# Kernel tuning notes

Hardware: AMD Instinct MI355X
Metric: run time of the kernel (lower is better)

The kernel has to match this reference:

```python
import jax, jax.numpy as jnp
import numpy as np

N = 16384          # nodes
E = 262144         # edges (avg degree 16)
MUL0, MUL1 = 16, 8 # multiplicities of 0e and 1o irreps
DIM = MUL0 + 3 * MUL1  # 40
NB, RH = 10, 16    # radial basis size, radial hidden
MAX_RADIUS = 1.3
W00_N = MUL0 * MUL0
W11_N = MUL1 * MUL0
W01_N = MUL0 * MUL1
W10_N = MUL1 * MUL1
WNUM = W00_N + W11_N + W01_N + W10_N  # 576
INV_SQRT3 = 1.0 / np.sqrt(3.0)        # wigner-3j (1,1,0) / (1,0,1) factor
A_PATH = 1.0 / np.sqrt(MUL0 + MUL1)   # path/fan normalization


def split_irreps(x):
    sc = x[..., :MUL0]
    vec = x[..., MUL0:].reshape(x.shape[:-1] + (MUL1, 3))
    return sc, vec


def radial_net(emb, w1, w2):
    h = jax.nn.silu(emb @ w1 / np.sqrt(NB))
    return h @ w2 / np.sqrt(RH)  # [E, WNUM]


def fc_tp(f_sc, f_vec, sh_sc, sh_vec, w):
    # fully-connected tensor product (input irreps x SH -> output irreps), per-edge weights
    w00 = w[:, :W00_N].reshape(-1, MUL0, MUL0)
    w11 = w[:, W00_N:W00_N + W11_N].reshape(-1, MUL1, MUL0)
    w01 = w[:, W00_N + W11_N:W00_N + W11_N + W01_N].reshape(-1, MUL0, MUL1)
    w10 = w[:, -W10_N:].reshape(-1, MUL1, MUL1)
    out_sc = A_PATH * (jnp.einsum('ei,e,eio->eo', f_sc, sh_sc, w00)
                       + INV_SQRT3 * jnp.einsum('eic,ec,eio->eo', f_vec, sh_vec, w11))
    out_vec = A_PATH * (jnp.einsum('ei,ec,eio->eoc', f_sc, sh_vec, w01)
                        + jnp.einsum('eic,e,eio->eoc', f_vec, sh_sc, w10))
    return out_sc, out_vec


def dot_tp(q_sc, q_vec, k_sc, k_vec, Wd00, Wd11):
    # FullyConnectedTensorProduct(query, key, '0e') with shared weights -> scalar per edge
    s0 = jnp.einsum('ei,ej,ij->e', q_sc, k_sc, Wd00) / MUL0
    s1 = jnp.einsum('eic,ejc,ij->e', q_vec, k_vec, Wd11) / (MUL1 * np.sqrt(3.0))
    return (s0 + s1) / np.sqrt(2.0)


def soft_unit_step(x):
    xs = jnp.where(x > 0, x, 1.0)
    return jnp.where(x > 0, jnp.exp(-1.0 / xs), 0.0)


def setup_inputs():
    key = jax.random.key(0)
    ks = jax.random.split(key, 13)
    return {
        'f': jax.random.normal(ks[0], (N, DIM), jnp.float32),
        'edge_index': jax.random.randint(ks[1], (2, E), 0, N),
        'edge_length': jax.random.uniform(ks[2], (E,), jnp.float32),
        'edge_sh': jax.random.normal(ks[3], (E, 4), jnp.float32),
        'edge_length_embedded': jax.random.uniform(ks[4], (E, NB), jnp.float32),
        'Wq0': jax.random.normal(ks[5], (MUL0, MUL0), jnp.float32),
        'Wq1': jax.random.normal(ks[6], (MUL1, MUL1), jnp.float32),
        'fck_w1': jax.random.normal(ks[7], (NB, RH), jnp.float32),
        'fck_w2': jax.random.normal(ks[8], (RH, WNUM), jnp.float32),
        'fcv_w1': jax.random.normal(ks[9], (NB, RH), jnp.float32),
        'fcv_w2': jax.random.normal(ks[10], (RH, WNUM), jnp.float32),
        'Wd00': jax.random.normal(ks[11], (MUL0, MUL0), jnp.float32),
        'Wd11': jax.random.normal(ks[12], (MUL1, MUL1), jnp.float32),
    }


def reference(f, edge_index, edge_length, edge_sh, edge_length_embedded,
              Wq0, Wq1, fck_w1, fck_w2, fcv_w1, fcv_w2, Wd00, Wd11):
    f_sc, f_vec = split_irreps(f)
    # h_q: equivariant linear (per-irrep channel mixing)
    q_sc = f_sc @ Wq0 / np.sqrt(MUL0)
    q_vec = jnp.einsum('nic,io->noc', f_vec, Wq1) / np.sqrt(MUL1)
    src, dst = edge_index[0], edge_index[1]
    sh_sc, sh_vec = edge_sh[:, 0], edge_sh[:, 1:4]
    # radial MLPs -> per-edge TP weights
    wk = radial_net(edge_length_embedded, fck_w1, fck_w2)
    wv = radial_net(edge_length_embedded, fcv_w1, fcv_w2)
    k_sc, k_vec = fc_tp(f_sc[dst], f_vec[dst], sh_sc, sh_vec, wk)
    v_sc, v_vec = fc_tp(f_sc[src], f_vec[src], sh_sc, sh_vec, wv)
    cut = soft_unit_step(10.0 * (1.0 - edge_length / MAX_RADIUS))
    s = dot_tp(q_sc[dst], q_vec[dst], k_sc, k_vec, Wd00, Wd11)
    exp_ijk = cut * jnp.exp(s)                                   # [E]
    z = jax.ops.segment_sum(exp_ijk, dst, num_segments=N)        # [N]
    z = jnp.where(z == 0, 1.0, z)
    alpha = exp_ijk / z[dst]
    w_edge = jnp.sqrt(jnp.maximum(alpha, 0.0))[:, None]          # sqrt(relu(alpha))
    v_flat = jnp.concatenate([v_sc, v_vec.reshape(-1, MUL1 * 3)], axis=-1)
    f_out = jax.ops.segment_sum(w_edge * v_flat, dst, num_segments=N)
    return f_out
```

## Files before the change

### kernel.cpp

```cpp
#include <hip/hip_runtime.h>
#include <hip/hip_bf16.h>
#include <math.h>

namespace {
constexpr int NN  = 16384;
constexpr int NE  = 262144;
constexpr int DIM = 40;

constexpr float INV_SQRT3   = 0.5773502691896258f;
constexpr float A_PATH      = 0.2041241452319315f;
constexpr float INV_SQRT_NB = 0.31622776601683794f;
constexpr float H_SCALE     = 0.25f;
constexpr float QSC_S       = 0.25f;
constexpr float QV_S        = 0.35355339059327373f;
constexpr float D00_S       = 1.0f / (16.0f * 1.4142135623730951f);
constexpr float D11_S       = 1.0f / (8.0f * 1.7320508075688772f * 1.4142135623730951f);

constexpr int BKP = 392;
constexpr int K0P = 328;
constexpr int KCP = 264;
constexpr int BKTOT = 16 * K0P + 16 * KCP;
constexpr int FEP = 40;

constexpr int PREP_NODE_BLKS = NN / 256;
constexpr int PREP_BV_BLKS   = 32 * BKP / 256;
constexpr int PREP_BK_BLKS   = BKTOT / 256;
}

typedef __attribute__((ext_vector_type(8))) _Float16 f16x8;
typedef __attribute__((ext_vector_type(4))) float f32x4;

static __device__ __forceinline__ void gload_lds16(const void* g, void* l) {
  __builtin_amdgcn_global_load_lds(
      (const __attribute__((address_space(1))) unsigned*)g,
      (__attribute__((address_space(3))) unsigned*)l, 16, 0, 0);
}

__global__ __launch_bounds__(256) void prep_kernel(
    const float* __restrict__ f,
    const float* __restrict__ Wq0, const float* __restrict__ Wq1,
    const float* __restrict__ Wd00, const float* __restrict__ Wd11,
    const float* __restrict__ w2v,
    const float* __restrict__ w2k,
    float* __restrict__ qd,
    unsigned short* __restrict__ Btv,
    unsigned short* __restrict__ Btk,
    int* __restrict__ cnt)
{
  const int blk = blockIdx.x;
  if (blk < PREP_NODE_BLKS) {
    const int n = blk * 256 + threadIdx.x;
    cnt[n] = 0;

    float fs[16], fv[8][3];
    {
      const float4* fn4 = reinterpret_cast<const float4*>(f + (size_t)n * DIM);
#pragma unroll
      for (int i = 0; i < 10; i++) {
        float4 t = fn4[i];
        int base = i * 4;
#pragma unroll
        for (int k = 0; k < 4; k++) {
          float v = (k == 0) ? t.x : (k == 1) ? t.y : (k == 2) ? t.z : t.w;
          int idx = base + k;
          if (idx < 16) fs[idx] = v;
          else { int r = idx - 16; fv[r / 3][r % 3] = v; }
        }
      }
    }

    float out[40];
    {
      float qsc[16];
#pragma unroll
      for (int o = 0; o < 16; o++) {
        float a = 0.f;
#pragma unroll
        for (int i = 0; i < 16; i++) a += fs[i] * Wq0[i * 16 + o];
        qsc[o] = a * QSC_S;
      }
#pragma unroll
      for (int j = 0; j < 16; j++) {
        float a = 0.f;
#pragma unroll
        for (int i = 0; i < 16; i++) a += qsc[i] * Wd00[i * 16 + j];
        out[j] = a * D00_S;
      }
    }
    {
      float qv[8][3];
#pragma unroll
      for (int o = 0; o < 8; o++)
#pragma unroll
        for (int c = 0; c < 3; c++) {
          float a = 0.f;
#pragma unroll
          for (int i = 0; i < 8; i++) a += fv[i][c] * Wq1[i * 8 + o];
          qv[o][c] = a * QV_S;
        }
#pragma unroll
      for (int j = 0; j < 8; j++)
#pragma unroll
        for (int c = 0; c < 3; c++) {
          float a = 0.f;
#pragma unroll
          for (int i = 0; i < 8; i++) a += qv[i][c] * Wd11[i * 8 + j];
          out[16 + j * 3 + c] = a * D11_S;
        }
    }

    float4* op = reinterpret_cast<float4*>(qd + (size_t)n * DIM);
#pragma unroll
    for (int i = 0; i < 10; i++)
      op[i] = make_float4(out[4 * i], out[4 * i + 1], out[4 * i + 2], out[4 * i + 3]);

  } else if (blk < PREP_NODE_BLKS + PREP_BV_BLKS) {
    int t = (blk - PREP_NODE_BLKS) * 256 + threadIdx.x;
    int col = t / BKP, kp = t % BKP;
    float val = 0.f;
    if (kp < 384 && col < 24) {
      if (kp < 256) {
        int r = kp >> 4, i = kp & 15;
        if (col < 16) val = A_PATH * w2v[r * 576 + i * 16 + col];
        else          val = A_PATH * w2v[r * 576 + 384 + i * 8 + (col - 16)];
      } else {
        int k2 = kp - 256; int r = k2 >> 3, i = k2 & 7;
        if (col < 16) val = A_PATH * INV_SQRT3 * w2v[r * 576 + 256 + i * 16 + col];
        else          val = A_PATH * w2v[r * 576 + 512 + i * 8 + (col - 16)];
      }
    }
    _Float16 hv = (_Float16)val;
    Btv[t] = __builtin_bit_cast(unsigned short, hv);

  } else {
    int t = (blk - PREP_NODE_BLKS - PREP_BV_BLKS) * 256 + threadIdx.x;
    float val = 0.f;
    if (t < 16 * K0P) {
      int r = t / K0P, k = t % K0P;
      if (k < 256)      { int i = k >> 4, o = k & 15; val = w2k[r * 576 + i * 16 + o]; }
      else if (k < 320) { int kk = k - 256; int i = kk >> 3, o = kk & 7;
                          val = w2k[r * 576 + 512 + i * 8 + o]; }
    } else {
      int t2 = t - 16 * K0P;
      int r = t2 / KCP, k = t2 % KCP;
      if (k < 128)      { int i = k >> 4, o = k & 15;
                          val = INV_SQRT3 * w2k[r * 576 + 256 + i * 16 + o]; }
      else if (k < 256) { int kk = k - 128; int i = kk >> 3, o = kk & 7;
                          val = w2k[r * 576 + 384 + i * 8 + o]; }
    }
    _Float16 hv = (_Float16)val;
    Btk[t] = __builtin_bit_cast(unsigned short, hv);
  }
}

__global__ __launch_bounds__(256) void qq_mfma_kernel(
    const float* __restrict__ f,
    const float* __restrict__ qd,
    const unsigned short* __restrict__ Btk,
    float* __restrict__ qq)
{
  __shared__ __attribute__((aligned(16))) unsigned short BL[BKTOT];
  __shared__ float fsT[16][65];
  __shared__ float fvT[24][65];
  __shared__ float qd0T[16][65];
  __shared__ float qdvT[24][65];

  const int tid  = threadIdx.x;
  const int base = blockIdx.x * 64;

  {
    const char* src = (const char*)Btk;
    char* dst = (char*)BL;
#pragma unroll
    for (int k2 = 0; k2 < 4; k2++) {
      int off = (k2 * 256 + tid) * 16;
      gload_lds16(src + off, dst + off);
    }
    if (tid < 160) {
      int off = (1024 + tid) * 16;
      gload_lds16(src + off, dst + off);
    }
  }

  const int m = tid & 63;
  const int q = tid >> 6;
  const int n = base + m;

  if (q == 0) {
    const float4* f4 = reinterpret_cast<const float4*>(f + (size_t)n * DIM);
    float v[40];
#pragma unroll
    for (int i = 0; i < 10; i++) {
      float4 t = f4[i];
      v[4 * i] = t.x; v[4 * i + 1] = t.y; v[4 * i + 2] = t.z; v[4 * i + 3] = t.w;
    }
#pragma unroll
    for (int i = 0; i < 16; i++) fsT[i][m] = v[i];
#pragma unroll
    for (int k = 0; k < 24; k++) fvT[(k % 3) * 8 + (k / 3)][m] = v[16 + k];
  } else if (q == 1) {
    const float4* q4 = reinterpret_cast<const float4*>(qd + (size_t)n * DIM);
    float v[40];
#pragma unroll
    for (int i = 0; i < 10; i++) {
      float4 t = q4[i];
      v[4 * i] = t.x; v[4 * i + 1] = t.y; v[4 * i + 2] = t.z; v[4 * i + 3] = t.w;
    }
#pragma unroll
    for (int i = 0; i < 16; i++) qd0T[i][m] = v[i];
#pragma unroll
    for (int k = 0; k < 24; k++) qdvT[(k % 3) * 8 + (k / 3)][m] = v[16 + k];
  }
  __syncthreads();

  const int w    = tid >> 6;
  const int l    = tid & 63;
  const int row  = l & 15;
  const int kb   = l >> 4;
  const int mrow = w * 16 + row;
  const int col  = l & 15;

  f32x4 p0  = {0.f, 0.f, 0.f, 0.f};
  f32x4 pcA = {0.f, 0.f, 0.f, 0.f}, pcB = {0.f, 0.f, 0.f, 0.f}, pcC = {0.f, 0.f, 0.f, 0.f};

#pragma unroll
  for (int s = 0; s < 10; s++) {
    f16x8 a;
    if (s < 8) {
      const int i  = 2 * s + (kb >> 1);
      const int o0 = (kb & 1) * 8;
      const float fsv = fsT[i][mrow];
#pragma unroll
      for (int j = 0; j < 8; j++) a[j] = (_Float16)(fsv * qd0T[o0 + j][mrow]);
    } else {
      const int i = (s - 8) * 4 + kb;
      const float fv0 = fvT[i][mrow], fv1 = fvT[8 + i][mrow], fv2 = fvT[16 + i][mrow];
#pragma unroll
      for (int j = 0; j < 8; j++)
        a[j] = (_Float16)(fv0 * qdvT[j][mrow] + fv1 * qdvT[8 + j][mrow]
                          + fv2 * qdvT[16 + j][mrow]);
    }
    const int k0 = s * 32 + kb * 8;
    f16x8 b = *reinterpret_cast<const f16x8*>(&BL[col * K0P + k0]);
    p0 = __builtin_amdgcn_mfma_f32_16x16x32_f16(a, b, p0, 0, 0, 0);
  }

#pragma unroll
  for (int c = 0; c < 3; c++) {
    f32x4* pc = (c == 0) ? &pcA : (c == 1) ? &pcB : &pcC;
#pragma unroll
    for (int s = 0; s < 8; s++) {
      f16x8 a;
      if (s < 4) {
        const int i  = 2 * s + (kb >> 1);
        const int o0 = (kb & 1) * 8;
        const float fvv = fvT[c * 8 + i][mrow];
#pragma unroll
        for (int j = 0; j < 8; j++) a[j] = (_Float16)(fvv * qd0T[o0 + j][mrow]);
      } else {
        const int i = (s - 4) * 4 + kb;
        const float fsv = fsT[i][mrow];
#pragma unroll
        for (int j = 0; j < 8; j++) a[j] = (_Float16)(fsv * qdvT[c * 8 + j][mrow]);
      }
      const int k0 = s * 32 + kb * 8;
      f16x8 b = *reinterpret_cast<const f16x8*>(&BL[16 * K0P + col * KCP + k0]);
      *pc = __builtin_amdgcn_mfma_f32_16x16x32_f16(a, b, *pc, 0, 0, 0);
    }
  }

#pragma unroll
  for (int j = 0; j < 4; j++) {
    const int me = w * 16 + kb * 4 + j;
    float4 outv = make_float4(A_PATH * p0[j], A_PATH * pcA[j],
                              A_PATH * pcB[j], A_PATH * pcC[j]);
    reinterpret_cast<float4*>(qq)[(size_t)(base + me) * 16 + col] = outv;
  }
}

__global__ __launch_bounds__(256) void hist_kernel(const int* __restrict__ ei,
                                                   int* __restrict__ cnt)
{
  const int e = blockIdx.x * 256 + threadIdx.x;
  atomicAdd(&cnt[ei[NE + e]], 1);
}

__global__ __launch_bounds__(1024) void scan_kernel(const int* __restrict__ cnt,
                                                    int* __restrict__ off,
                                                    float* __restrict__ z)
{
  __shared__ int part[1024];
  const int t = threadIdx.x;
  const int base = t * 16;
  int loc[16];
  int s = 0;
#pragma unroll
  for (int k = 0; k < 16; k++) { loc[k] = s; s += cnt[base + k]; }
  part[t] = s;
  __syncthreads();
  for (int d = 1; d < 1024; d <<= 1) {
    int v = (t >= d) ? part[t - d] : 0;
    __syncthreads();
    part[t] += v;
    __syncthreads();
  }
  int excl = (t == 0) ? 0 : part[t - 1];
#pragma unroll
  for (int k = 0; k < 16; k++) {
    off[base + k] = excl + loc[k];
    z[base + k] = 0.f;
  }
}

__global__ __launch_bounds__(256) void scatter_kernel(const int* __restrict__ ei,
                                                      int* __restrict__ off,
                                                      int* __restrict__ eperm,
                                                      int* __restrict__ dst_sorted,
                                                      float* __restrict__ out)
{
  const int gid = blockIdx.x * 256 + threadIdx.x;
#pragma unroll
  for (int i = 0; i < 3; i++) {
    int idx = gid + i * NE;
    if (idx < NN * DIM) out[idx] = 0.f;
  }
  const int dst = ei[NE + gid];
  int rk = atomicAdd(&off[dst], 1);
  eperm[rk] = gid;
  dst_sorted[rk] = dst;
}

__global__ __launch_bounds__(256) void k_pass_kernel(
    const int*   __restrict__ eperm,
    const int*   __restrict__ dst_sorted,
    const float* __restrict__ elen,
    const float* __restrict__ esh,
    const float* __restrict__ emb,
    const float* __restrict__ w1,
    const float* __restrict__ qq,
    float* __restrict__ expv,
    float* __restrict__ z)
{
  const int rk = blockIdx.x * 256 + threadIdx.x;
  const int e = eperm[rk];
  const int dst = dst_sorted[rk];

  float el[10];
  const float2* e2 = reinterpret_cast<const float2*>(emb + (size_t)e * 10);
#pragma unroll
  for (int b = 0; b < 5; b++) { float2 t = e2[b]; el[2 * b] = t.x; el[2 * b + 1] = t.y; }

  float h[16];
#pragma unroll
  for (int j = 0; j < 16; j++) {
    float a = 0.f;
#pragma unroll
    for (int b = 0; b < 10; b++) a += el[b] * w1[b * 16 + j];
    a *= INV_SQRT_NB;
    float sig = 1.0f / (1.0f + __expf(-a));
    h[j] = a * sig * H_SCALE;
  }

  float4 sh4 = reinterpret_cast<const float4*>(esh)[e];
  const float4* q4 = reinterpret_cast<const float4*>(qq + (size_t)dst * 64);
  float s = 0.f;
#pragma unroll
  for (int r = 0; r < 16; r++) {
    float4 qv = q4[r];
    s += h[r] * (sh4.x * qv.x + sh4.y * qv.y + sh4.z * qv.z + sh4.w * qv.w);
  }

  float len = elen[e];
  float x = 10.0f * (1.0f - len * (1.0f / 1.3f));
  float cut = (x > 0.f) ? __expf(-1.0f / x) : 0.f;
  float ev = cut * __expf(s);
  expv[rk] = ev;
  atomicAdd(&z[dst], ev);
}

__global__ __launch_bounds__(256) void v_mfma_kernel(
    const int*   __restrict__ ei,
    const float* __restrict__ esh,
    const float* __restrict__ emb,
    const float* __restrict__ w1,
    const float* __restrict__ f,
    const float* __restrict__ expv,
    const float* __restrict__ z,
    const int*   __restrict__ eperm,
    const int*   __restrict__ dst_sorted,
    const unsigned short* __restrict__ Bt,
    float* __restrict__ fout)
{
  __shared__ float h_s[64][17];
  __shared__ __attribute__((aligned(16))) _Float16 feE[64][FEP];
  __shared__ float scal[64][5];
  __shared__ int   nid[64];
  __shared__ __attribute__((aligned(16))) unsigned short BtL[32][BKP];
  __shared__ float rows[64][41];
  __shared__ int seg_start[64], seg_len[64], seg_nid[64];
  __shared__ int nseg_s;

  const int tid  = threadIdx.x;
  const int base = blockIdx.x * 64;

  {
    const char* src = (const char*)Bt;
    char* dst = (char*)&BtL[0][0];
#pragma unroll
    for (int k = 0; k < 6; k++) {
      int off = (k * 256 + tid) * 16;
      gload_lds16(src + off, dst + off);
    }
    if (tid < 32) {
      int off = (1536 + tid) * 16;
      gload_lds16(src + off, dst + off);
    }
  }

  const int m = tid & 63;
  const int q = tid >> 6;
  const int e = eperm[base + m];

  if (q == 0) {
    int dn = dst_sorted[base + m];
    float4 sh4 = reinterpret_cast<const float4*>(esh)[e];
    float zz = z[dn]; zz = (zz == 0.f) ? 1.f : zz;
    float ev = expv[base + m];
    float wgt = sqrtf(fmaxf(ev / zz, 0.f));
    scal[m][0] = sh4.x; scal[m][1] = sh4.y; scal[m][2] = sh4.z; scal[m][3] = sh4.w;
    scal[m][4] = wgt;
    nid[m] = dn;
  } else if (q == 3) {
    int sn = ei[e];
    const float4* f4 = reinterpret_cast<const float4*>(f + (size_t)sn * DIM);
    float v[40];
#pragma unroll
    for (int i = 0; i < 10; i++) {
      float4 t = f4[i];
      v[4 * i] = t.x; v[4 * i + 1] = t.y; v[4 * i + 2] = t.z; v[4 * i + 3] = t.w;
    }
#pragma unroll
    for (int i = 0; i < 16; i++) feE[m][i] = (_Float16)v[i];
#pragma unroll
    for (int k = 0; k < 24; k++)
      feE[m][16 + (k % 3) * 8 + (k / 3)] = (_Float16)v[16 + k];
  } else {
    float el[10];
    const float2* e2 = reinterpret_cast<const float2*>(emb + (size_t)e * 10);
#pragma unroll
    for (int b = 0; b < 5; b++) { float2 t = e2[b]; el[2 * b] = t.x; el[2 * b + 1] = t.y; }
    const int j0 = (q == 1) ? 0 : 8;
#pragma unroll
    for (int jj = 0; jj < 8; jj++) {
      int j = j0 + jj;
      float a = 0.f;
#pragma unroll
      for (int b = 0; b < 10; b++) a += el[b] * w1[b * 16 + j];
      a *= INV_SQRT_NB;
      float sig = 1.0f / (1.0f + __expf(-a));
      h_s[m][j] = a * sig * H_SCALE;
    }
  }
  __syncthreads();

  const int w    = tid >> 6;
  const int l    = tid & 63;
  const int row  = l & 15;
  const int kb   = l >> 4;
  const int mrow = w * 16 + row;
  const int col  = l & 15;

  const int i0 = (kb & 1) * 8;
  f16x8 afs = *reinterpret_cast<const f16x8*>(&feE[mrow][i0]);
  f16x8 afv0 = *reinterpret_cast<const f16x8*>(&feE[mrow][16]);
  f16x8 afv1 = *reinterpret_cast<const f16x8*>(&feE[mrow][24]);
  f16x8 afv2 = *reinterpret_cast<const f16x8*>(&feE[mrow][32]);

  f32x4 pfs0 = {0.f, 0.f, 0.f, 0.f}, pfs1 = {0.f, 0.f, 0.f, 0.f};
  f32x4 pc0_0 = {0.f, 0.f, 0.f, 0.f}, pc0_1 = {0.f, 0.f, 0.f, 0.f}, pc0_2 = {0.f, 0.f, 0.f, 0.f};
  f32x4 pc1_0 = {0.f, 0.f, 0.f, 0.f}, pc1_1 = {0.f, 0.f, 0.f, 0.f}, pc1_2 = {0.f, 0.f, 0.f, 0.f};

#pragma unroll
  for (int s = 0; s < 8; s++) {
    const int r  = 2 * s + (kb >> 1);
    const _Float16 hr = (_Float16)h_s[mrow][r];
    f16x8 a;
#pragma unroll
    for (int j = 0; j < 8; j++) a[j] = hr * afs[j];
    const int k0 = s * 32 + kb * 8;
    f16x8 b0 = *reinterpret_cast<const f16x8*>(&BtL[col][k0]);
    f16x8 b1 = *reinterpret_cast<const f16x8*>(&BtL[16 + col][k0]);
    pfs0 = __builtin_amdgcn_mfma_f32_16x16x32_f16(a, b0, pfs0, 0, 0, 0);
    pfs1 = __builtin_amdgcn_mfma_f32_16x16x32_f16(a, b1, pfs1, 0, 0, 0);
  }

#pragma unroll
  for (int s = 0; s < 4; s++) {
    const int r = 4 * s + kb;
    const _Float16 hr = (_Float16)h_s[mrow][r];
    const int k0 = 256 + s * 32 + kb * 8;
    f16x8 b0 = *reinterpret_cast<const f16x8*>(&BtL[col][k0]);
    f16x8 b1 = *reinterpret_cast<const f16x8*>(&BtL[16 + col][k0]);
#pragma unroll
    for (int c = 0; c < 3; c++) {
      const f16x8 av = (c == 0) ? afv0 : (c == 1) ? afv1 : afv2;
      f16x8 a;
#pragma unroll
      for (int j = 0; j < 8; j++) a[j] = hr * av[j];
      f32x4* p0 = (c == 0) ? &pc0_0 : (c == 1) ? &pc0_1 : &pc0_2;
      f32x4* p1 = (c == 0) ? &pc1_0 : (c == 1) ? &pc1_1 : &pc1_2;
      *p0 = __builtin_amdgcn_mfma_f32_16x16x32_f16(a, b0, *p0, 0, 0, 0);
      *p1 = __builtin_amdgcn_mfma_f32_16x16x32_f16(a, b1, *p1, 0, 0, 0);
    }
  }

#pragma unroll
  for (int j = 0; j < 4; j++) {
    const int me = w * 16 + kb * 4 + j;
    const float sh0 = scal[me][0], sh1 = scal[me][1], sh2 = scal[me][2], sh3 = scal[me][3];
    const float wg = scal[me][4];
    float vsc = sh0 * pfs0[j] + sh1 * pc0_0[j] + sh2 * pc0_1[j] + sh3 * pc0_2[j];
    rows[me][col] = wg * vsc;
    if (col < 8) {
      rows[me][16 + col * 3 + 0] = wg * (sh1 * pfs1[j] + sh0 * pc1_0[j]);
      rows[me][16 + col * 3 + 1] = wg * (sh2 * pfs1[j] + sh0 * pc1_1[j]);
      rows[me][16 + col * 3 + 2] = wg * (sh3 * pfs1[j] + sh0 * pc1_2[j]);
    }
  }
  __syncthreads();

  if (tid < 64) {
    bool head = (m == 0) || (nid[m] != nid[m - 1]);
    unsigned long long mask = __ballot(head);
    if (tid == 0) nseg_s = __popcll(mask);
    if (head) {
      int idx = __popcll(mask & ((1ull << m) - 1ull));
      unsigned long long higher = (m == 63) ? 0ull : (mask >> (m + 1));
      int len = higher ? __ffsll((long long)higher) : (64 - m);
      seg_start[idx] = m; seg_len[idx] = len; seg_nid[idx] = nid[m];
    }
  }
  __syncthreads();

  const int nseg = nseg_s;
  const int d = tid & 63;
  const int g = tid >> 6;
  if (d < DIM) {
    for (int s = g; s < nseg; s += 4) {
      const int st = seg_start[s], ln = seg_len[s];
      float acc = 0.f;
      for (int k2 = 0; k2 < ln; k2++) acc += rows[st + k2][d];
      float* fo = &fout[(size_t)seg_nid[s] * DIM + d];
      if (s > 0 && s < nseg - 1) *fo = acc;
      else atomicAdd(fo, acc);
    }
  }
}

extern "C" void kernel_launch(void* const* d_in, const int* in_sizes, int n_in,
                              void* d_out, int out_size, void* d_ws, size_t ws_size,
                              hipStream_t stream) {
  const float* f      = (const float*)d_in[0];
  const int*   ei     = (const int*)d_in[1];
  const float* elen   = (const float*)d_in[2];
  const float* esh    = (const float*)d_in[3];
  const float* emb    = (const float*)d_in[4];
  const float* Wq0    = (const float*)d_in[5];
  const float* Wq1    = (const float*)d_in[6];
  const float* fck_w1 = (const float*)d_in[7];
  const float* fck_w2 = (const float*)d_in[8];
  const float* fcv_w1 = (const float*)d_in[9];
  const float* fcv_w2 = (const float*)d_in[10];
  const float* Wd00   = (const float*)d_in[11];
  const float* Wd11   = (const float*)d_in[12];

  float* out = (float*)d_out;

  char* ws = (char*)d_ws;
  float* qq     = (float*)ws;  ws += (size_t)NN * 64 * 4;
  float* qd     = (float*)ws;  ws += (size_t)NN * DIM * 4;
  float* z      = (float*)ws;  ws += (size_t)NN * 4;
  float* expv   = (float*)ws;  ws += (size_t)NE * 4;
  int*   cnt    = (int*)ws;    ws += (size_t)NN * 4;
  int*   off    = (int*)ws;    ws += (size_t)NN * 4;
  int*   eperm  = (int*)ws;    ws += (size_t)NE * 4;
  int*   dsts   = (int*)ws;    ws += (size_t)NE * 4;
  unsigned short* Btv = (unsigned short*)ws;  ws += (size_t)32 * BKP * 2;
  unsigned short* Btk = (unsigned short*)ws;  ws += (size_t)BKTOT * 2;

  prep_kernel<<<PREP_NODE_BLKS + PREP_BV_BLKS + PREP_BK_BLKS, 256, 0, stream>>>(
      f, Wq0, Wq1, Wd00, Wd11, fcv_w2, fck_w2, qd, Btv, Btk, cnt);
  hist_kernel<<<NE / 256, 256, 0, stream>>>(ei, cnt);
  scan_kernel<<<1, 1024, 0, stream>>>(cnt, off, z);
  qq_mfma_kernel<<<NN / 64, 256, 0, stream>>>(f, qd, Btk, qq);
  scatter_kernel<<<NE / 256, 256, 0, stream>>>(ei, off, eperm, dsts, out);
  k_pass_kernel<<<NE / 256, 256, 0, stream>>>(eperm, dsts, elen, esh, emb,
                                              fck_w1, qq, expv, z);
  v_mfma_kernel<<<NE / 64, 256, 0, stream>>>(ei, esh, emb, fcv_w1, f, expv, z,
                                             eperm, dsts, Btv, out);
}
```

Measured before the change: 122.9 us.

## Fuse scatter and key pass into edge kernel; precompute value radial hidden in rank order

```diff
diff --git a/kernel.cpp b/kernel.cpp
--- a/kernel.cpp
+++ b/kernel.cpp
@@ -312,11 +312,22 @@
   }
 }
 
-__global__ __launch_bounds__(256) void scatter_kernel(const int* __restrict__ ei,
-                                                      int* __restrict__ off,
-                                                      int* __restrict__ eperm,
-                                                      int* __restrict__ dst_sorted,
-                                                      float* __restrict__ out)
+__global__ __launch_bounds__(256) void edge_kernel(
+    const int*   __restrict__ ei,
+    const float* __restrict__ elen,
+    const float* __restrict__ esh,
+    const float* __restrict__ emb,
+    const float* __restrict__ w1k,
+    const float* __restrict__ w1v,
+    const float* __restrict__ qq,
+    int*   __restrict__ off,
+    int*   __restrict__ dsts,
+    int*   __restrict__ srcs,
+    float* __restrict__ esh_rank,
+    _Float16* __restrict__ hv_rank,
+    float* __restrict__ expv,
+    float* __restrict__ z,
+    float* __restrict__ out)
 {
   const int gid = blockIdx.x * 256 + threadIdx.x;
 #pragma unroll
@@ -324,29 +335,13 @@
     int idx = gid + i * NE;
     if (idx < NN * DIM) out[idx] = 0.f;
   }
+
+  const int src = ei[gid];
   const int dst = ei[NE + gid];
-  int rk = atomicAdd(&off[dst], 1);
-  eperm[rk] = gid;
-  dst_sorted[rk] = dst;
-}
-
-__global__ __launch_bounds__(256) void k_pass_kernel(
-    const int*   __restrict__ eperm,
-    const int*   __restrict__ dst_sorted,
-    const float* __restrict__ elen,
-    const float* __restrict__ esh,
-    const float* __restrict__ emb,
-    const float* __restrict__ w1,
-    const float* __restrict__ qq,
-    float* __restrict__ expv,
-    float* __restrict__ z)
-{
-  const int rk = blockIdx.x * 256 + threadIdx.x;
-  const int e = eperm[rk];
-  const int dst = dst_sorted[rk];
+  const int rk = atomicAdd(&off[dst], 1);
 
   float el[10];
-  const float2* e2 = reinterpret_cast<const float2*>(emb + (size_t)e * 10);
+  const float2* e2 = reinterpret_cast<const float2*>(emb + (size_t)gid * 10);
 #pragma unroll
   for (int b = 0; b < 5; b++) { float2 t = e2[b]; el[2 * b] = t.x; el[2 * b + 1] = t.y; }
 
@@ -355,13 +350,13 @@
   for (int j = 0; j < 16; j++) {
     float a = 0.f;
 #pragma unroll
-    for (int b = 0; b < 10; b++) a += el[b] * w1[b * 16 + j];
+    for (int b = 0; b < 10; b++) a += el[b] * w1k[b * 16 + j];
     a *= INV_SQRT_NB;
     float sig = 1.0f / (1.0f + __expf(-a));
     h[j] = a * sig * H_SCALE;
   }
 
-  float4 sh4 = reinterpret_cast<const float4*>(esh)[e];
+  float4 sh4 = reinterpret_cast<const float4*>(esh)[gid];
   const float4* q4 = reinterpret_cast<const float4*>(qq + (size_t)dst * 64);
   float s = 0.f;
 #pragma unroll
@@ -370,24 +365,41 @@
     s += h[r] * (sh4.x * qv.x + sh4.y * qv.y + sh4.z * qv.z + sh4.w * qv.w);
   }
 
-  float len = elen[e];
+  float len = elen[gid];
   float x = 10.0f * (1.0f - len * (1.0f / 1.3f));
   float cut = (x > 0.f) ? __expf(-1.0f / x) : 0.f;
   float ev = cut * __expf(s);
   expv[rk] = ev;
   atomicAdd(&z[dst], ev);
+
+  f16x8 hv0, hv1;
+#pragma unroll
+  for (int j = 0; j < 16; j++) {
+    float a = 0.f;
+#pragma unroll
+    for (int b = 0; b < 10; b++) a += el[b] * w1v[b * 16 + j];
+    a *= INV_SQRT_NB;
+    float sig = 1.0f / (1.0f + __expf(-a));
+    _Float16 hh = (_Float16)(a * sig * H_SCALE);
+    if (j < 8) hv0[j] = hh; else hv1[j - 8] = hh;
+  }
+  f16x8* hvp = reinterpret_cast<f16x8*>(hv_rank + (size_t)rk * 16);
+  hvp[0] = hv0;
+  hvp[1] = hv1;
+
+  dsts[rk] = dst;
+  srcs[rk] = src;
+  reinterpret_cast<float4*>(esh_rank)[rk] = sh4;
 }
 
 __global__ __launch_bounds__(256) void v_mfma_kernel(
-    const int*   __restrict__ ei,
-    const float* __restrict__ esh,
-    const float* __restrict__ emb,
-    const float* __restrict__ w1,
     const float* __restrict__ f,
     const float* __restrict__ expv,
     const float* __restrict__ z,
-    const int*   __restrict__ eperm,
-    const int*   __restrict__ dst_sorted,
+    const int*   __restrict__ dsts,
+    const int*   __restrict__ srcs,
+    const float* __restrict__ esh_rank,
+    const _Float16* __restrict__ hv_rank,
     const unsigned short* __restrict__ Bt,
     float* __restrict__ fout)
 {
@@ -419,11 +431,10 @@
 
   const int m = tid & 63;
   const int q = tid >> 6;
-  const int e = eperm[base + m];
 
   if (q == 0) {
-    int dn = dst_sorted[base + m];
-    float4 sh4 = reinterpret_cast<const float4*>(esh)[e];
+    int dn = dsts[base + m];
+    float4 sh4 = reinterpret_cast<const float4*>(esh_rank)[base + m];
     float zz = z[dn]; zz = (zz == 0.f) ? 1.f : zz;
     float ev = expv[base + m];
     float wgt = sqrtf(fmaxf(ev / zz, 0.f));
@@ -431,7 +442,7 @@
     scal[m][4] = wgt;
     nid[m] = dn;
   } else if (q == 3) {
-    int sn = ei[e];
+    int sn = srcs[base + m];
     const float4* f4 = reinterpret_cast<const float4*>(f + (size_t)sn * DIM);
     float v[40];
 #pragma unroll
@@ -444,21 +455,13 @@
 #pragma unroll
     for (int k = 0; k < 24; k++)
       feE[m][16 + (k % 3) * 8 + (k / 3)] = (_Float16)v[16 + k];
-  } else {
-    float el[10];
-    const float2* e2 = reinterpret_cast<const float2*>(emb + (size_t)e * 10);
-#pragma unroll
-    for (int b = 0; b < 5; b++) { float2 t = e2[b]; el[2 * b] = t.x; el[2 * b + 1] = t.y; }
-    const int j0 = (q == 1) ? 0 : 8;
-#pragma unroll
-    for (int jj = 0; jj < 8; jj++) {
-      int j = j0 + jj;
-      float a = 0.f;
-#pragma unroll
-      for (int b = 0; b < 10; b++) a += el[b] * w1[b * 16 + j];
-      a *= INV_SQRT_NB;
-      float sig = 1.0f / (1.0f + __expf(-a));
-      h_s[m][j] = a * sig * H_SCALE;
+  } else if (q == 1) {
+    const f16x8* hp = reinterpret_cast<const f16x8*>(hv_rank + (size_t)(base + m) * 16);
+    f16x8 h0 = hp[0], h1 = hp[1];
+#pragma unroll
+    for (int j = 0; j < 8; j++) {
+      h_s[m][j]     = (float)h0[j];
+      h_s[m][8 + j] = (float)h1[j];
     }
   }
   __syncthreads();
@@ -577,14 +580,16 @@
   float* out = (float*)d_out;
 
   char* ws = (char*)d_ws;
-  float* qq     = (float*)ws;  ws += (size_t)NN * 64 * 4;
-  float* qd     = (float*)ws;  ws += (size_t)NN * DIM * 4;
-  float* z      = (float*)ws;  ws += (size_t)NN * 4;
-  float* expv   = (float*)ws;  ws += (size_t)NE * 4;
-  int*   cnt    = (int*)ws;    ws += (size_t)NN * 4;
-  int*   off    = (int*)ws;    ws += (size_t)NN * 4;
-  int*   eperm  = (int*)ws;    ws += (size_t)NE * 4;
-  int*   dsts   = (int*)ws;    ws += (size_t)NE * 4;
+  float* qq       = (float*)ws;  ws += (size_t)NN * 64 * 4;
+  float* qd       = (float*)ws;  ws += (size_t)NN * DIM * 4;
+  float* z        = (float*)ws;  ws += (size_t)NN * 4;
+  float* expv     = (float*)ws;  ws += (size_t)NE * 4;
+  int*   cnt      = (int*)ws;    ws += (size_t)NN * 4;
+  int*   off      = (int*)ws;    ws += (size_t)NN * 4;
+  int*   dsts     = (int*)ws;    ws += (size_t)NE * 4;
+  int*   srcs     = (int*)ws;    ws += (size_t)NE * 4;
+  float* esh_rank = (float*)ws;  ws += (size_t)NE * 4 * 4;
+  _Float16* hv_rank = (_Float16*)ws;  ws += (size_t)NE * 16 * 2;
   unsigned short* Btv = (unsigned short*)ws;  ws += (size_t)32 * BKP * 2;
   unsigned short* Btk = (unsigned short*)ws;  ws += (size_t)BKTOT * 2;
 
@@ -593,9 +598,9 @@
   hist_kernel<<<NE / 256, 256, 0, stream>>>(ei, cnt);
   scan_kernel<<<1, 1024, 0, stream>>>(cnt, off, z);
   qq_mfma_kernel<<<NN / 64, 256, 0, stream>>>(f, qd, Btk, qq);
-  scatter_kernel<<<NE / 256, 256, 0, stream>>>(ei, off, eperm, dsts, out);
-  k_pass_kernel<<<NE / 256, 256, 0, stream>>>(eperm, dsts, elen, esh, emb,
-                                              fck_w1, qq, expv, z);
-  v_mfma_kernel<<<NE / 64, 256, 0, stream>>>(ei, esh, emb, fcv_w1, f, expv, z,
-                                             eperm, dsts, Btv, out);
-}
+  edge_kernel<<<NE / 256, 256, 0, stream>>>(ei, elen, esh, emb, fck_w1, fcv_w1,
+                                            qq, off, dsts, srcs, esh_rank,
+                                            hv_rank, expv, z, out);
+  v_mfma_kernel<<<NE / 64, 256, 0, stream>>>(f, expv, z, dsts, srcs, esh_rank,
+                                             hv_rank, Btv, out);
+}
```

After: 108.1 us. -12.1%, faster.
